# Kernel tuning notes

Hardware: AMD Instinct MI355X
Metric: run time of the kernel (lower is better)

The kernel has to match this reference:

```python
import jax, jax.numpy as jnp
import numpy as np

B, S, D, H, DK = 2, 2048, 1024, 16, 64  # batch, seq, d_model, heads, head_dim


def setup_inputs() -> dict:
    key = jax.random.key(0)
    ks = jax.random.split(key, 11)
    inp = {
        "v": jax.random.normal(ks[0], (B, S, D), dtype=jnp.float32),
        "k": jax.random.normal(ks[1], (B, S, D), dtype=jnp.float32),
        "q": jax.random.normal(ks[2], (B, S, D), dtype=jnp.float32),
        # per-head Linear(d_model, d_k): torch weight shape [d_k, d_model], stacked over heads
        "Wq": jax.random.normal(ks[3], (H, DK, D), dtype=jnp.float32) * 0.02,
        "bq": jax.random.normal(ks[4], (H, DK), dtype=jnp.float32) * 0.02,
        "Wk": jax.random.normal(ks[5], (H, DK, D), dtype=jnp.float32) * 0.02,
        "bk": jax.random.normal(ks[6], (H, DK), dtype=jnp.float32) * 0.02,
        "Wv": jax.random.normal(ks[7], (H, DK, D), dtype=jnp.float32) * 0.02,
        "bv": jax.random.normal(ks[8], (H, DK), dtype=jnp.float32) * 0.02,
        "Wo": jax.random.normal(ks[9], (D, D), dtype=jnp.float32) * 0.02,
        "bo": jax.random.normal(ks[10], (D,), dtype=jnp.float32) * 0.02,
    }
    return inp


def reference(v, k, q, Wq, bq, Wk, bk, Wv, bv, Wo, bo):
    # Batched per-head projections (original uses a python loop over h Linears).
    # torch Linear: y = x @ W.T + b  ->  einsum over last dim of W.
    q2 = jnp.einsum("bsd,hkd->bhsk", q, Wq) + bq[None, :, None, :]
    k2 = jnp.einsum("bsd,hkd->bhsk", k, Wk) + bk[None, :, None, :]
    v2 = jnp.einsum("bsd,hkd->bhsk", v, Wv) + bv[None, :, None, :]
    # FAITHFUL to source bug: attention(v2, k2, q2) -> scores from v2 @ k2^T,
    # softmax, then weighted sum of q2. (dropout = identity in eval mode)
    scores = jnp.einsum("bhsk,bhtk->bhst", v2, k2) / jnp.sqrt(jnp.float32(DK))
    attn = jax.nn.softmax(scores, axis=-1)
    out = jnp.einsum("bhst,bhtk->bhsk", attn, q2)
    # concat heads in order (head i -> slice [i*d_k:(i+1)*d_k])
    out = out.transpose(0, 2, 1, 3).reshape(B, S, H * DK)
    return out @ Wo.T + bo
```

## Files before the change

kernel.cpp:

```cpp
#include <hip/hip_runtime.h>
#include <stdint.h>

#define B_  2
#define S_  2048
#define D_  1024
#define H_  16
#define DK_ 64
#define VST 2176

typedef unsigned short u16;
typedef short bf16x8 __attribute__((ext_vector_type(8)));
typedef float f32x4  __attribute__((ext_vector_type(4)));

#define MFMA(a,b,c) __builtin_amdgcn_mfma_f32_16x16x32_bf16((a),(b),(c),0,0,0)
#define EXP2(x) __builtin_amdgcn_exp2f(x)

static __device__ __forceinline__ u16 f2bf(float f) {
    uint32_t u = __float_as_uint(f);
    u += 0x7fffu + ((u >> 16) & 1u);
    return (u16)(u >> 16);
}
static __device__ __forceinline__ uint32_t pk2(float x, float y) {
    return __builtin_amdgcn_perm(__float_as_uint(y) + 0x8000u,
                                 __float_as_uint(x) + 0x8000u, 0x07060302u);
}

typedef const __attribute__((address_space(1))) void* gas_p;
typedef __attribute__((address_space(3))) void* las_p;
static __device__ __forceinline__ void gld16(const void* g, void* l) {
    __builtin_amdgcn_global_load_lds((gas_p)g, (las_p)l, 16, 0, 0);
}


__global__ void conv_all(const float* __restrict__ v, const float* __restrict__ k,
                         const float* __restrict__ q,
                         const float* __restrict__ Wv, const float* __restrict__ Wk,
                         const float* __restrict__ Wq, const float* __restrict__ Wo,
                         u16* __restrict__ dst) {
    const int b = blockIdx.x;
    const float* s;
    size_t loc, segbase;
    if (b < 12288) {
        const int t = b >> 12;
        s = (t == 0) ? v : (t == 1 ? k : q);
        segbase = (size_t)t * 4194304;
        loc = (size_t)(b & 4095) * 1024;
    } else {
        const int t = (b - 12288) >> 10;
        s = (t == 0) ? Wv : (t == 1 ? Wk : (t == 2 ? Wq : Wo));
        segbase = 12582912 + (size_t)t * 1048576;
        loc = (size_t)(b & 1023) * 1024;
    }
    loc += threadIdx.x * 4;
    float4 f = *(const float4*)(s + loc);
    ushort4 o;
    o.x = f2bf(f.x); o.y = f2bf(f.y); o.z = f2bf(f.z); o.w = f2bf(f.w);
    *(ushort4*)(dst + segbase + loc) = o;
}


__global__ __launch_bounds__(256) void proj_gemm(
    const u16* __restrict__ Xb, const u16* __restrict__ Wb,
    const float* __restrict__ bv, const float* __restrict__ bk, const float* __restrict__ bq,
    u16* __restrict__ v2, u16* __restrict__ k2, u16* __restrict__ q2T)
{
    __shared__ alignas(16) char smem[40960];
    u16* lA = (u16*)smem;
    u16* lB = (u16*)(smem + 16384);
    u16* epi = (u16*)smem;

    const int z = blockIdx.z;
    const u16* A = Xb + (size_t)z * 4194304;
    const u16* W = Wb + (size_t)z * 1048576;
    const float* bias = (z == 0) ? bv : (z == 1 ? bk : bq);

    const int tid = threadIdx.x;
    const int lane = tid & 63, wave = tid >> 6;
    const int wm = wave >> 1, wn = wave & 1;
    const int q = lane >> 4, l15 = lane & 15;
    const int q4 = q * 4;

    const int f = blockIdx.y * 8 + blockIdx.x;
    const int rowbase = (f & 31) * 128;
    const int colbase = (f >> 5) * 128;

    const int srow = wave * 8 + (lane >> 3);
    const int cg = (lane & 7) ^ (lane >> 3);
    const u16* gA = A + (size_t)(rowbase + srow) * D_ + cg * 8;
    const u16* gW = W + (size_t)(colbase + srow) * D_ + cg * 8;
    u16* lAp = lA + wave * 512 + lane * 8;
    u16* lBp = lB + wave * 512 + lane * 8;

    const int sw = l15 & 7;
    const int fo0 = (q ^ sw) * 8;
    const int fo1 = fo0 ^ 32;

    f32x4 acc[4][4] = {};

    for (int k0 = 0; k0 < D_; k0 += 64) {
        #pragma unroll
        for (int j = 0; j < 4; j++) {
            gld16(gA + k0 + (size_t)j * 32 * D_, lAp + j * 2048);
            gld16(gW + k0 + (size_t)j * 32 * D_, lBp + j * 2048);
        }
        __syncthreads();
        bf16x8 a0[4], a1[4], b0[4], b1[4];
        #pragma unroll
        for (int mi = 0; mi < 4; mi++) {
            const int r = (wm * 64 + mi * 16 + l15) * 64;
            a0[mi] = *(const bf16x8*)&lA[r + fo0];
            a1[mi] = *(const bf16x8*)&lA[r + fo1];
        }
        #pragma unroll
        for (int ni = 0; ni < 4; ni++) {
            const int r = (wn * 64 + ni * 16 + l15) * 64;
            b0[ni] = *(const bf16x8*)&lB[r + fo0];
            b1[ni] = *(const bf16x8*)&lB[r + fo1];
        }
        #pragma unroll
        for (int mi = 0; mi < 4; mi++)
            #pragma unroll
            for (int ni = 0; ni < 4; ni++) {
                acc[mi][ni] = MFMA(a0[mi], b0[ni], acc[mi][ni]);
                acc[mi][ni] = MFMA(a1[mi], b1[ni], acc[mi][ni]);
            }
        __syncthreads();
    }

    u16* ep = epi + wave * (64 * 80);
    const int h = (colbase + wn * 64) >> 6;
    const int Mrow0 = rowbase + wm * 64;
    const int bb = Mrow0 >> 11;

    if (z < 2) {
        u16* outp = (z == 0) ? v2 : k2;
        const float scale = (z == 0) ? 0.18033688011112042f : 1.0f;
        #pragma unroll
        for (int mi = 0; mi < 4; mi++)
            #pragma unroll
            for (int ni = 0; ni < 4; ni++) {
                const float bc = bias[colbase + wn * 64 + ni * 16 + l15];
                #pragma unroll
                for (int rg = 0; rg < 4; rg++)
                    ep[(mi * 16 + q4 + rg) * 80 + ni * 16 + l15] =
                        f2bf((acc[mi][ni][rg] + bc) * scale);
            }
        asm volatile("s_waitcnt lgkmcnt(0)" ::: "memory");
        const int s = (Mrow0 + lane) & (S_ - 1);
        u16* gb = outp + ((size_t)(bb * H_ + h) * S_ + s) * DK_;
        #pragma unroll
        for (int j = 0; j < 8; j++)
            *(uint4*)(gb + j * 8) = *(const uint4*)&ep[lane * 80 + j * 8];
    } else {
        #pragma unroll
        for (int mi = 0; mi < 4; mi++)
            #pragma unroll
            for (int ni = 0; ni < 4; ni++) {
                const float bc = bias[colbase + wn * 64 + ni * 16 + l15];
                uint2 pk;
                pk.x = pk2(acc[mi][ni][0] + bc, acc[mi][ni][1] + bc);
                pk.y = pk2(acc[mi][ni][2] + bc, acc[mi][ni][3] + bc);
                *(uint2*)&ep[(ni * 16 + l15) * 80 + mi * 16 + q4] = pk;
            }
        asm volatile("s_waitcnt lgkmcnt(0)" ::: "memory");
        const int s0g = Mrow0 & (S_ - 1);
        u16* gb = q2T + ((size_t)(bb * H_ + h) * DK_ + lane) * VST + s0g;
        #pragma unroll
        for (int j = 0; j < 8; j++)
            *(uint4*)(gb + j * 8) = *(const uint4*)&ep[lane * 80 + j * 8];
    }
}


__global__ __launch_bounds__(256) void flash_attn(
    const u16* __restrict__ v2, const u16* __restrict__ k2,
    const u16* __restrict__ q2T, u16* __restrict__ Ob)
{
    __shared__ alignas(16) u16 lK[2][64 * 64];
    __shared__ alignas(16) u16 lV[2][64 * 64];
    __shared__ alignas(16) u16 ldsP[4][2][16][68];

    const int tid = threadIdx.x;
    const int lane = tid & 63, wave = tid >> 6;
    const int q = lane >> 4, l15 = lane & 15;
    const int q4 = q * 4;
    const int bh = blockIdx.x & 31;
    const int sbase = (blockIdx.x >> 5) * 128;

    const u16* Qp = v2  + (size_t)bh * S_ * DK_;
    const u16* Kp = k2  + (size_t)bh * S_ * DK_;
    const u16* Vp = q2T + (size_t)bh * DK_ * VST;

    const int srow8 = lane >> 3;
    const int cs    = lane & 7;
    const int cg    = cs ^ srow8;
    const int krow0 = wave * 16 + srow8;

    bf16x8 bq[2][2];
    #pragma unroll
    for (int g = 0; g < 2; g++) {
        const u16* qp = Qp + (size_t)(sbase + g * 64 + wave * 16 + l15) * DK_ + q * 8;
        bq[g][0] = *(const bf16x8*)(qp);
        bq[g][1] = *(const bf16x8*)(qp + 32);
    }

    bf16x8 ones;
    #pragma unroll
    for (int i = 0; i < 8; i++) ones[i] = (short)0x3F80;

    f32x4 o_acc[2][4] = {};
    f32x4 o_l[2] = {};

    const int sw = l15 & 7;
    const int fc0 = (q ^ sw) * 8;
    const int fc1 = fc0 ^ 32;

    {
        const u16* kg = Kp + (size_t)krow0 * DK_ + cg * 8;
        const u16* vg = Vp + (size_t)krow0 * VST + cg * 8;
        u16* lkd = &lK[0][(wave * 128) * 8 + lane * 8];
        u16* lvd = &lV[0][(wave * 128) * 8 + lane * 8];
        gld16(kg, lkd);
        gld16(kg + 8 * DK_, lkd + 64 * 8);
        gld16(vg, lvd);
        gld16(vg + (size_t)8 * VST, lvd + 64 * 8);
    }

    for (int it = 0; it < S_ / 64; ++it) {
        const int buf = it & 1;
        __syncthreads();
        if (it + 1 < S_ / 64) {
            const int nb = (it + 1) & 1;
            const int t1 = (it + 1) * 64;
            const u16* kg = Kp + (size_t)(t1 + krow0) * DK_ + cg * 8;
            const u16* vg = Vp + (size_t)krow0 * VST + t1 + cg * 8;
            u16* lkd = &lK[nb][(wave * 128) * 8 + lane * 8];
            u16* lvd = &lV[nb][(wave * 128) * 8 + lane * 8];
            gld16(kg, lkd);
            gld16(kg + 8 * DK_, lkd + 64 * 8);
            gld16(vg, lvd);
            gld16(vg + (size_t)8 * VST, lvd + 64 * 8);
        }

        f32x4 s_acc[2][4];
        #pragma unroll
        for (int mi = 0; mi < 4; mi++) {
            const int trow = mi * 16 + l15;
            bf16x8 a0 = *(const bf16x8*)&lK[buf][trow * 64 + fc0];
            bf16x8 a1 = *(const bf16x8*)&lK[buf][trow * 64 + fc1];
            #pragma unroll
            for (int g = 0; g < 2; g++) {
                f32x4 zz = {};
                zz = MFMA(a0, bq[g][0], zz);
                s_acc[g][mi] = MFMA(a1, bq[g][1], zz);
            }
        }

        #pragma unroll
        for (int g = 0; g < 2; g++)
            #pragma unroll
            for (int mi = 0; mi < 4; mi++) {
                float p0 = EXP2(s_acc[g][mi][0]);
                float p1 = EXP2(s_acc[g][mi][1]);
                float p2 = EXP2(s_acc[g][mi][2]);
                float p3 = EXP2(s_acc[g][mi][3]);
                uint2 pk;
                pk.x = __builtin_amdgcn_perm(__float_as_uint(p1), __float_as_uint(p0), 0x07060302u);
                pk.y = __builtin_amdgcn_perm(__float_as_uint(p3), __float_as_uint(p2), 0x07060302u);
                *(uint2*)&ldsP[wave][g][l15][mi * 16 + q4] = pk;
            }

        asm volatile("s_waitcnt lgkmcnt(0)" ::: "memory");

        bf16x8 bp[2][2];
        #pragma unroll
        for (int g = 0; g < 2; g++) {
            uint2* r0 = (uint2*)&bp[g][0];
            r0[0] = *(const uint2*)&ldsP[wave][g][l15][q * 8];
            r0[1] = *(const uint2*)&ldsP[wave][g][l15][q * 8 + 4];
            uint2* r1 = (uint2*)&bp[g][1];
            r1[0] = *(const uint2*)&ldsP[wave][g][l15][32 + q * 8];
            r1[1] = *(const uint2*)&ldsP[wave][g][l15][32 + q * 8 + 4];
        }

        #pragma unroll
        for (int mi = 0; mi < 4; mi++) {
            const int dkrow = mi * 16 + l15;
            bf16x8 av0 = *(const bf16x8*)&lV[buf][dkrow * 64 + fc0];
            bf16x8 av1 = *(const bf16x8*)&lV[buf][dkrow * 64 + fc1];
            #pragma unroll
            for (int g = 0; g < 2; g++) {
                o_acc[g][mi] = MFMA(av0, bp[g][0], o_acc[g][mi]);
                o_acc[g][mi] = MFMA(av1, bp[g][1], o_acc[g][mi]);
            }
        }
        #pragma unroll
        for (int g = 0; g < 2; g++) {
            o_l[g] = MFMA(ones, bp[g][0], o_l[g]);
            o_l[g] = MFMA(ones, bp[g][1], o_l[g]);
        }

        asm volatile("s_barrier" ::: "memory");
    }

    const int bb = bh >> 4, h = bh & 15;
    #pragma unroll
    for (int g = 0; g < 2; g++) {
        const float inv_l = 1.0f / o_l[g][0];
        const int s = sbase + g * 64 + wave * 16 + l15;
        #pragma unroll
        for (int mi = 0; mi < 4; mi++) {
            ushort4 o4;
            o4.x = f2bf(o_acc[g][mi][0] * inv_l);
            o4.y = f2bf(o_acc[g][mi][1] * inv_l);
            o4.z = f2bf(o_acc[g][mi][2] * inv_l);
            o4.w = f2bf(o_acc[g][mi][3] * inv_l);
            *(ushort4*)(Ob + (size_t)(bb * S_ + s) * (H_ * DK_) + h * DK_ + mi * 16 + q4) = o4;
        }
    }
}


__global__ __launch_bounds__(256) void out_gemm(
    const u16* __restrict__ Ob, const u16* __restrict__ Wob,
    const float* __restrict__ bo, float* __restrict__ out)
{
    __shared__ alignas(16) u16 lA[128 * 64];
    __shared__ alignas(16) u16 lB[64 * 64];

    const int tid = threadIdx.x;
    const int lane = tid & 63, wave = tid >> 6;
    const int wm = wave >> 1, wn = wave & 1;
    const int q = lane >> 4, l15 = lane & 15;
    const int q4 = q * 4;

    const int f = blockIdx.y * 16 + blockIdx.x;
    const int rowbase = (f & 31) * 128;
    const int colbase = (f >> 5) * 64;

    const int srow = wave * 8 + (lane >> 3);
    const int cg = (lane & 7) ^ (lane >> 3);
    const u16* gA = Ob  + (size_t)(rowbase + srow) * D_ + cg * 8;
    const u16* gW = Wob + (size_t)(colbase + srow) * D_ + cg * 8;
    u16* lAp = lA + wave * 512 + lane * 8;
    u16* lBp = lB + wave * 512 + lane * 8;

    const int sw = l15 & 7;
    const int fo0 = (q ^ sw) * 8;
    const int fo1 = fo0 ^ 32;

    f32x4 acc[4][2] = {};

    for (int k0 = 0; k0 < D_; k0 += 64) {
        #pragma unroll
        for (int j = 0; j < 4; j++)
            gld16(gA + k0 + (size_t)j * 32 * D_, lAp + j * 2048);
        #pragma unroll
        for (int j = 0; j < 2; j++)
            gld16(gW + k0 + (size_t)j * 32 * D_, lBp + j * 2048);
        __syncthreads();
        bf16x8 a0[4], a1[4], b0[2], b1[2];
        #pragma unroll
        for (int mi = 0; mi < 4; mi++) {
            const int r = (wm * 64 + mi * 16 + l15) * 64;
            a0[mi] = *(const bf16x8*)&lA[r + fo0];
            a1[mi] = *(const bf16x8*)&lA[r + fo1];
        }
        #pragma unroll
        for (int ni = 0; ni < 2; ni++) {
            const int r = (wn * 32 + ni * 16 + l15) * 64;
            b0[ni] = *(const bf16x8*)&lB[r + fo0];
            b1[ni] = *(const bf16x8*)&lB[r + fo1];
        }
        #pragma unroll
        for (int mi = 0; mi < 4; mi++)
            #pragma unroll
            for (int ni = 0; ni < 2; ni++) {
                acc[mi][ni] = MFMA(a0[mi], b0[ni], acc[mi][ni]);
                acc[mi][ni] = MFMA(a1[mi], b1[ni], acc[mi][ni]);
            }
        __syncthreads();
    }

    #pragma unroll
    for (int mi = 0; mi < 4; mi++)
        #pragma unroll
        for (int ni = 0; ni < 2; ni++) {
            const int c = colbase + wn * 32 + ni * 16 + l15;
            const float bc = bo[c];
            #pragma unroll
            for (int rg = 0; rg < 4; rg++) {
                const int r = rowbase + wm * 64 + mi * 16 + q4 + rg;
                out[(size_t)r * D_ + c] = acc[mi][ni][rg] + bc;
            }
        }
}


extern "C" void kernel_launch(void* const* d_in, const int* in_sizes, int n_in,
                              void* d_out, int out_size, void* d_ws, size_t ws_size,
                              hipStream_t stream) {
    const float* v  = (const float*)d_in[0];
    const float* k  = (const float*)d_in[1];
    const float* qq = (const float*)d_in[2];
    const float* Wq = (const float*)d_in[3];
    const float* bq = (const float*)d_in[4];
    const float* Wk = (const float*)d_in[5];
    const float* bk = (const float*)d_in[6];
    const float* Wv = (const float*)d_in[7];
    const float* bv = (const float*)d_in[8];
    const float* Wo = (const float*)d_in[9];
    const float* bo = (const float*)d_in[10];
    float* out = (float*)d_out;

    char* w = (char*)d_ws;
    u16* cvtb = (u16*)w;
    u16* v2  = (u16*)(w + 33554432);
    u16* k2  = (u16*)(w + 41943040);
    u16* q2T = (u16*)(w + 50331648);
    u16* Ob  = (u16*)(w + 59244544);

    conv_all<<<16384, 256, 0, stream>>>(v, k, qq, Wv, Wk, Wq, Wo, cvtb);
    proj_gemm<<<dim3(8, 32, 3), 256, 0, stream>>>(cvtb, cvtb + 12582912,
                                                  bv, bk, bq, v2, k2, q2T);
    flash_attn<<<512, 256, 0, stream>>>(v2, k2, q2T, Ob);
    out_gemm<<<dim3(16, 32), 256, 0, stream>>>(Ob, cvtb + 15728640, bo, out);
}
```

Baseline: 226.5 us.

## Split attention key range across two wave groups and merge partial outputs in LDS

The flash attention kernel now runs 512-thread blocks covering 256 query rows. The two 4-wave halves each process half of the key/value sequence, and their unnormalized partial sums and row sums are combined through shared memory before the final write. Each wave now handles 64 query rows and reuses its per-tile K/V register loads across four query groups, which cuts LDS reads per MFMA. The exchange costs extra LDS space (about 81KB), a final reduction step, and higher register pressure, and the grid shrinks to 256 blocks, which may underfill the GPU.

```diff
diff --git a/kernel.cpp b/kernel.cpp
--- a/kernel.cpp
+++ b/kernel.cpp
@@ -172,20 +172,25 @@
 }
 
 
-__global__ __launch_bounds__(256) void flash_attn(
+__global__ __launch_bounds__(512, 2) void flash_attn(
     const u16* __restrict__ v2, const u16* __restrict__ k2,
     const u16* __restrict__ q2T, u16* __restrict__ Ob)
 {
-    __shared__ alignas(16) u16 lK[2][64 * 64];
-    __shared__ alignas(16) u16 lV[2][64 * 64];
-    __shared__ alignas(16) u16 ldsP[4][2][16][68];
+    __shared__ alignas(16) char smem[82944];
+    u16* lK   = (u16*)smem;
+    u16* lV   = (u16*)(smem + 32768);
+    u16* ldsP = (u16*)(smem + 65536);
+    float* Xo = (float*)smem;
+    float* Xl = (float*)(smem + 69632);
 
     const int tid = threadIdx.x;
     const int lane = tid & 63, wave = tid >> 6;
+    const int th = wave >> 2, wl = wave & 3;
     const int q = lane >> 4, l15 = lane & 15;
     const int q4 = q * 4;
     const int bh = blockIdx.x & 31;
-    const int sbase = (blockIdx.x >> 5) * 128;
+    const int sbase = (blockIdx.x >> 5) * 256;
+    const int tbase = th * 1024;
 
     const u16* Qp = v2  + (size_t)bh * S_ * DK_;
     const u16* Kp = k2  + (size_t)bh * S_ * DK_;
@@ -194,12 +199,14 @@
     const int srow8 = lane >> 3;
     const int cs    = lane & 7;
     const int cg    = cs ^ srow8;
-    const int krow0 = wave * 16 + srow8;
-
-    bf16x8 bq[2][2];
+    const int krow0 = wl * 16 + srow8;
+    u16* lKh = lK + th * 8192;
+    u16* lVh = lV + th * 8192;
+
+    bf16x8 bq[4][2];
     #pragma unroll
-    for (int g = 0; g < 2; g++) {
-        const u16* qp = Qp + (size_t)(sbase + g * 64 + wave * 16 + l15) * DK_ + q * 8;
+    for (int g = 0; g < 4; g++) {
+        const u16* qp = Qp + (size_t)(sbase + wl * 64 + g * 16 + l15) * DK_ + q * 8;
         bq[g][0] = *(const bf16x8*)(qp);
         bq[g][1] = *(const bf16x8*)(qp + 32);
     }
@@ -208,114 +215,122 @@
     #pragma unroll
     for (int i = 0; i < 8; i++) ones[i] = (short)0x3F80;
 
-    f32x4 o_acc[2][4] = {};
-    f32x4 o_l[2] = {};
+    f32x4 o_acc[4][4] = {};
+    f32x4 o_l[4] = {};
 
     const int sw = l15 & 7;
     const int fc0 = (q ^ sw) * 8;
     const int fc1 = fc0 ^ 32;
 
     {
-        const u16* kg = Kp + (size_t)krow0 * DK_ + cg * 8;
-        const u16* vg = Vp + (size_t)krow0 * VST + cg * 8;
-        u16* lkd = &lK[0][(wave * 128) * 8 + lane * 8];
-        u16* lvd = &lV[0][(wave * 128) * 8 + lane * 8];
+        const u16* kg = Kp + (size_t)(tbase + krow0) * DK_ + cg * 8;
+        const u16* vg = Vp + (size_t)krow0 * VST + tbase + cg * 8;
+        u16* lkd = lKh + wl * 1024 + lane * 8;
+        u16* lvd = lVh + wl * 1024 + lane * 8;
         gld16(kg, lkd);
-        gld16(kg + 8 * DK_, lkd + 64 * 8);
+        gld16(kg + 8 * DK_, lkd + 512);
         gld16(vg, lvd);
-        gld16(vg + (size_t)8 * VST, lvd + 64 * 8);
-    }
-
-    for (int it = 0; it < S_ / 64; ++it) {
+        gld16(vg + (size_t)8 * VST, lvd + 512);
+    }
+
+    u16* Pw = ldsP + wave * (16 * 68);
+
+    for (int it = 0; it < 16; ++it) {
         const int buf = it & 1;
         __syncthreads();
-        if (it + 1 < S_ / 64) {
-            const int nb = (it + 1) & 1;
-            const int t1 = (it + 1) * 64;
+        if (it + 1 < 16) {
+            const int t1 = tbase + (it + 1) * 64;
             const u16* kg = Kp + (size_t)(t1 + krow0) * DK_ + cg * 8;
             const u16* vg = Vp + (size_t)krow0 * VST + t1 + cg * 8;
-            u16* lkd = &lK[nb][(wave * 128) * 8 + lane * 8];
-            u16* lvd = &lV[nb][(wave * 128) * 8 + lane * 8];
+            u16* lkd = lKh + (buf ^ 1) * 4096 + wl * 1024 + lane * 8;
+            u16* lvd = lVh + (buf ^ 1) * 4096 + wl * 1024 + lane * 8;
             gld16(kg, lkd);
-            gld16(kg + 8 * DK_, lkd + 64 * 8);
+            gld16(kg + 8 * DK_, lkd + 512);
             gld16(vg, lvd);
-            gld16(vg + (size_t)8 * VST, lvd + 64 * 8);
-        }
-
-        f32x4 s_acc[2][4];
+            gld16(vg + (size_t)8 * VST, lvd + 512);
+        }
+
+        const u16* Kt = lKh + buf * 4096;
+        const u16* Vt = lVh + buf * 4096;
+        bf16x8 ak0[4], ak1[4], av0[4], av1[4];
         #pragma unroll
         for (int mi = 0; mi < 4; mi++) {
-            const int trow = mi * 16 + l15;
-            bf16x8 a0 = *(const bf16x8*)&lK[buf][trow * 64 + fc0];
-            bf16x8 a1 = *(const bf16x8*)&lK[buf][trow * 64 + fc1];
-            #pragma unroll
-            for (int g = 0; g < 2; g++) {
+            const int r = (mi * 16 + l15) * 64;
+            ak0[mi] = *(const bf16x8*)&Kt[r + fc0];
+            ak1[mi] = *(const bf16x8*)&Kt[r + fc1];
+            av0[mi] = *(const bf16x8*)&Vt[r + fc0];
+            av1[mi] = *(const bf16x8*)&Vt[r + fc1];
+        }
+
+        #pragma unroll
+        for (int g = 0; g < 4; g++) {
+            f32x4 sa[4];
+            #pragma unroll
+            for (int mi = 0; mi < 4; mi++) {
                 f32x4 zz = {};
-                zz = MFMA(a0, bq[g][0], zz);
-                s_acc[g][mi] = MFMA(a1, bq[g][1], zz);
-            }
-        }
-
-        #pragma unroll
-        for (int g = 0; g < 2; g++)
+                zz = MFMA(ak0[mi], bq[g][0], zz);
+                sa[mi] = MFMA(ak1[mi], bq[g][1], zz);
+            }
             #pragma unroll
             for (int mi = 0; mi < 4; mi++) {
-                float p0 = EXP2(s_acc[g][mi][0]);
-                float p1 = EXP2(s_acc[g][mi][1]);
-                float p2 = EXP2(s_acc[g][mi][2]);
-                float p3 = EXP2(s_acc[g][mi][3]);
+                float p0 = EXP2(sa[mi][0]);
+                float p1 = EXP2(sa[mi][1]);
+                float p2 = EXP2(sa[mi][2]);
+                float p3 = EXP2(sa[mi][3]);
                 uint2 pk;
                 pk.x = __builtin_amdgcn_perm(__float_as_uint(p1), __float_as_uint(p0), 0x07060302u);
                 pk.y = __builtin_amdgcn_perm(__float_as_uint(p3), __float_as_uint(p2), 0x07060302u);
-                *(uint2*)&ldsP[wave][g][l15][mi * 16 + q4] = pk;
-            }
-
-        asm volatile("s_waitcnt lgkmcnt(0)" ::: "memory");
-
-        bf16x8 bp[2][2];
-        #pragma unroll
-        for (int g = 0; g < 2; g++) {
-            uint2* r0 = (uint2*)&bp[g][0];
-            r0[0] = *(const uint2*)&ldsP[wave][g][l15][q * 8];
-            r0[1] = *(const uint2*)&ldsP[wave][g][l15][q * 8 + 4];
-            uint2* r1 = (uint2*)&bp[g][1];
-            r1[0] = *(const uint2*)&ldsP[wave][g][l15][32 + q * 8];
-            r1[1] = *(const uint2*)&ldsP[wave][g][l15][32 + q * 8 + 4];
-        }
-
-        #pragma unroll
-        for (int mi = 0; mi < 4; mi++) {
-            const int dkrow = mi * 16 + l15;
-            bf16x8 av0 = *(const bf16x8*)&lV[buf][dkrow * 64 + fc0];
-            bf16x8 av1 = *(const bf16x8*)&lV[buf][dkrow * 64 + fc1];
-            #pragma unroll
-            for (int g = 0; g < 2; g++) {
-                o_acc[g][mi] = MFMA(av0, bp[g][0], o_acc[g][mi]);
-                o_acc[g][mi] = MFMA(av1, bp[g][1], o_acc[g][mi]);
-            }
-        }
-        #pragma unroll
-        for (int g = 0; g < 2; g++) {
-            o_l[g] = MFMA(ones, bp[g][0], o_l[g]);
-            o_l[g] = MFMA(ones, bp[g][1], o_l[g]);
-        }
-
-        asm volatile("s_barrier" ::: "memory");
-    }
-
-    const int bb = bh >> 4, h = bh & 15;
-    #pragma unroll
-    for (int g = 0; g < 2; g++) {
-        const float inv_l = 1.0f / o_l[g][0];
-        const int s = sbase + g * 64 + wave * 16 + l15;
-        #pragma unroll
-        for (int mi = 0; mi < 4; mi++) {
-            ushort4 o4;
-            o4.x = f2bf(o_acc[g][mi][0] * inv_l);
-            o4.y = f2bf(o_acc[g][mi][1] * inv_l);
-            o4.z = f2bf(o_acc[g][mi][2] * inv_l);
-            o4.w = f2bf(o_acc[g][mi][3] * inv_l);
-            *(ushort4*)(Ob + (size_t)(bb * S_ + s) * (H_ * DK_) + h * DK_ + mi * 16 + q4) = o4;
+                *(uint2*)&Pw[l15 * 68 + mi * 16 + q4] = pk;
+            }
+            asm volatile("s_waitcnt lgkmcnt(0)" ::: "memory");
+            bf16x8 bp0, bp1;
+            {
+                uint2* r0 = (uint2*)&bp0;
+                r0[0] = *(const uint2*)&Pw[l15 * 68 + q * 8];
+                r0[1] = *(const uint2*)&Pw[l15 * 68 + q * 8 + 4];
+                uint2* r1 = (uint2*)&bp1;
+                r1[0] = *(const uint2*)&Pw[l15 * 68 + 32 + q * 8];
+                r1[1] = *(const uint2*)&Pw[l15 * 68 + 32 + q * 8 + 4];
+            }
+            #pragma unroll
+            for (int mi = 0; mi < 4; mi++) {
+                o_acc[g][mi] = MFMA(av0[mi], bp0, o_acc[g][mi]);
+                o_acc[g][mi] = MFMA(av1[mi], bp1, o_acc[g][mi]);
+            }
+            o_l[g] = MFMA(ones, bp0, o_l[g]);
+            o_l[g] = MFMA(ones, bp1, o_l[g]);
+        }
+    }
+
+    __syncthreads();
+    if (th == 1) {
+        #pragma unroll
+        for (int g = 0; g < 4; g++) {
+            const int sr = wl * 64 + g * 16 + l15;
+            #pragma unroll
+            for (int mi = 0; mi < 4; mi++)
+                *(f32x4*)&Xo[sr * 68 + mi * 16 + q4] = o_acc[g][mi];
+            if (q == 0) Xl[sr] = o_l[g][0];
+        }
+    }
+    __syncthreads();
+    if (th == 0) {
+        const int bb = bh >> 4, h = bh & 15;
+        #pragma unroll
+        for (int g = 0; g < 4; g++) {
+            const int sr = wl * 64 + g * 16 + l15;
+            const float inv_l = 1.0f / (o_l[g][0] + Xl[sr]);
+            const int s = sbase + sr;
+            #pragma unroll
+            for (int mi = 0; mi < 4; mi++) {
+                f32x4 p = *(const f32x4*)&Xo[sr * 68 + mi * 16 + q4];
+                ushort4 o4;
+                o4.x = f2bf((o_acc[g][mi][0] + p[0]) * inv_l);
+                o4.y = f2bf((o_acc[g][mi][1] + p[1]) * inv_l);
+                o4.z = f2bf((o_acc[g][mi][2] + p[2]) * inv_l);
+                o4.w = f2bf((o_acc[g][mi][3] + p[3]) * inv_l);
+                *(ushort4*)(Ob + (size_t)(bb * S_ + s) * (H_ * DK_) + h * DK_ + mi * 16 + q4) = o4;
+            }
         }
     }
 }
@@ -423,6 +438,6 @@
     conv_all<<<16384, 256, 0, stream>>>(v, k, qq, Wv, Wk, Wq, Wo, cvtb);
     proj_gemm<<<dim3(8, 32, 3), 256, 0, stream>>>(cvtb, cvtb + 12582912,
                                                   bv, bk, bq, v2, k2, q2T);
-    flash_attn<<<512, 256, 0, stream>>>(v2, k2, q2T, Ob);
+    flash_attn<<<256, 512, 0, stream>>>(v2, k2, q2T, Ob);
     out_gemm<<<dim3(16, 32), 256, 0, stream>>>(Ob, cvtb + 15728640, bo, out);
 }
```

After: 216.7 us. 1.04x faster.
